# Performance work log

Measured on AMD Instinct MI355X. Metric: run time of the kernel, lower is better.

The kernel has to match this reference:

```python
import jax, jax.numpy as jnp
import numpy as np

N, E, D, H = 10000, 160000, 128, 8


def setup_inputs() -> dict:
    key = jax.random.key(0)
    ks = jax.random.split(key, 12)
    s = 0.05  # xavier-ish init scale
    return {
        "x": jax.random.normal(ks[0], (N, D), jnp.float32),
        "conn_ex": jax.random.normal(ks[1], (E, D), jnp.float32),
        "edge_index": jax.random.randint(ks[2], (2, E), 0, N),
        "sqrt_deg": jax.random.uniform(ks[3], (N, 1), jnp.float32, 0.5, 2.0),
        "qkv_w": (jax.random.normal(ks[4], (3 * D, D)) * s).astype(jnp.float32),
        "qkv_b": jnp.zeros((3 * D,), jnp.float32),
        "w1": (jax.random.normal(ks[5], (2 * D, D)) * s).astype(jnp.float32),
        "b1": jnp.zeros((2 * D,), jnp.float32),
        "wscore": (jax.random.normal(ks[6], (D // H, H, 1)) * s).astype(jnp.float32),
        "w2": (jax.random.normal(ks[7], (D, D)) * s).astype(jnp.float32),
        "b2": jnp.zeros((D,), jnp.float32),
        "bn_c_g": jnp.ones((D,), jnp.float32),
        "bn_c_b": jnp.zeros((D,), jnp.float32),
        "deg_coef": (jax.random.normal(ks[8], (1, D, 2)) * s).astype(jnp.float32),
        "ffn1_w": (jax.random.normal(ks[9], (2 * D, D)) * s).astype(jnp.float32),
        "ffn1_b": jnp.zeros((2 * D,), jnp.float32),
        "ffn2_w": (jax.random.normal(ks[10], (D, 2 * D)) * s).astype(jnp.float32),
        "ffn2_b": jnp.zeros((D,), jnp.float32),
        "bn1_g": jnp.ones((D,), jnp.float32),
        "bn1_b": jnp.zeros((D,), jnp.float32),
        "bn2_g": jnp.ones((D,), jnp.float32),
        "bn2_b": jnp.zeros((D,), jnp.float32),
        "num_nodes": N,
    }


def _bn(v, g, b):
    # BatchNorm1d, training-mode statistics (biased variance), eps=1e-5
    mu = v.mean(0)
    var = v.var(0)
    return (v - mu) / jnp.sqrt(var + 1e-5) * g + b


def _seg_softmax(s, idx, n):
    # sparse softmax over segments of dim 0 given by idx (pyg_softmax)
    m = jax.ops.segment_max(s, idx, num_segments=n)
    e = jnp.exp(s - m[idx])
    den = jax.ops.segment_sum(e, idx, num_segments=n)[idx] + 1e-16
    return e / den


def reference(x, conn_ex, edge_index, sqrt_deg, qkv_w, qkv_b, w1, b1, wscore,
              w2, b2, bn_c_g, bn_c_b, deg_coef, ffn1_w, ffn1_b, ffn2_w, ffn2_b,
              bn1_g, bn1_b, bn2_g, bn2_b, num_nodes):
    n, d = x.shape
    h = wscore.shape[1]
    dh = d // h
    # packed QKV projection
    qkv = x @ qkv_w.T + qkv_b
    Q, K, V = qkv[:, :d], qkv[:, d:2 * d], qkv[:, 2 * d:]
    dst, src = edge_index[0], edge_index[1]
    e = dst.shape[0]
    # edge-conditioned weights/bias: conn_lin1 output split into (Ew, Eb)
    Eh = conn_ex @ w1.T + b1  # [E, 2d]
    Ew, Eb = Eh[:, :d], Eh[:, d:]
    c = (Q[dst] + K[src]) * Ew
    # sqrt(relu(c)) - sqrt(relu(-c)) == sign(c)*sqrt(|c|) (signed sqrt)
    c = jnp.sign(c) * jnp.sqrt(jnp.abs(c)) + Eb
    c = jax.nn.relu(c)  # act; dropout p=0
    c2 = jax.nn.relu(_bn(c @ w2.T + b2 + conn_ex, bn_c_g, bn_c_b))  # [E, d]
    # attention scores per head
    score = jnp.einsum('ehd,dhc->ehc', c.reshape(e, h, dh), wscore)  # [E,H,1]
    score = jnp.clip(score, -5.0, 5.0)
    alpha = _seg_softmax(score, dst, num_nodes)  # [E,H,1]
    # scatter-add aggregation of weighted V and conn features
    nagg = jax.ops.segment_sum(V[src].reshape(e, h, dh) * alpha, dst, num_segments=num_nodes)
    cagg = jax.ops.segment_sum(c2.reshape(e, h, dh) * alpha, dst, num_segments=num_nodes)
    nh = (nagg + cagg).reshape(n, d)
    # degree rescaling
    nh = (jnp.stack([nh, nh * sqrt_deg], axis=-1) * deg_coef).sum(-1)
    h_res = nh + x
    nh = _bn(h_res, bn1_g, bn1_b)
    nh = jax.nn.relu(nh @ ffn1_w.T + ffn1_b) @ ffn2_w.T + ffn2_b
    nh = _bn(nh + h_res, bn2_g, bn2_b)
    return nh, c2
```

## Files before the change

### kernel.cpp

```cpp
#include <hip/hip_runtime.h>
#include <math.h>

typedef float f4 __attribute__((ext_vector_type(4)));
typedef float f2 __attribute__((ext_vector_type(2)));
typedef short bf16x8 __attribute__((ext_vector_type(8)));
typedef float f32x4v __attribute__((ext_vector_type(4)));
typedef unsigned short u16x4 __attribute__((ext_vector_type(4)));

#define N_NODES 10000
#define N_EDGES 160000

#define OFF_DEN     0
#define OFF_SUMS    80000
#define OFF_DEG     80768
#define ZERO_WORDS  90768
#define OFF_ROWPTR  90768
#define OFF_CURSOR  100772
#define OFF_ELIST   110772
#define OFF_SS      270772
#define OFF_QKV     271544
#define OFF_ESC     4111544
#define OFF_HRES    5391544
#define OFF_Y       6671544
#define OFF_MID     7951544
#define OFF_WBF     10511544

__device__ __forceinline__ unsigned short f2bf(float f) {
  unsigned int u = __float_as_uint(f);
  u = (u + 0x7fffu + ((u >> 16) & 1u)) >> 16;
  return (unsigned short)u;
}
__device__ __forceinline__ float bf2f(unsigned short p) {
  return __uint_as_float(((unsigned int)p) << 16);
}

__global__ void k_cvt(const float* __restrict__ w1, const float* __restrict__ w2,
                      unsigned short* __restrict__ w1bf,
                      unsigned short* __restrict__ w2bf) {
  int i = blockIdx.x * 256 + threadIdx.x;
  if (i < 32768) w1bf[i] = f2bf(w1[i]);
  if (i < 16384) w2bf[i] = f2bf(w2[i]);
}

__global__ __launch_bounds__(256, 4) void k_edge(
    const float* __restrict__ conn, const int* __restrict__ ei,
    const float* __restrict__ qkv, const unsigned short* __restrict__ w1bf,
    const unsigned short* __restrict__ w2bf, const float* __restrict__ b1,
    const float* __restrict__ b2, const float* __restrict__ wsc_g,
    float* __restrict__ t_out, float* __restrict__ escore,
    float* __restrict__ den, float* __restrict__ bnc_sums) {
  __shared__ unsigned short connBF[8192];
  __shared__ unsigned short qkcBF[8192];
  __shared__ float scoreAcc[64][8];
  __shared__ float wscS[128];
  __shared__ float csum[128], csq[128];
  const int tid = threadIdx.x;
  const int e0 = blockIdx.x * 64;

  if (tid < 128) { wscS[tid] = wsc_g[tid]; csum[tid] = 0.f; }
  else { csq[tid - 128] = 0.f; }

#pragma unroll
  for (int it = 0; it < 8; ++it) {
    int i = tid + it * 256;
    int row = i >> 5, kq = i & 31;
    int wb = ((row * 256 + kq * 8) ^ ((row & 7) << 4)) >> 1;
    f4 cv = *(const f4*)&conn[(e0 + row) * 128 + kq * 4];
    u16x4 cp = { f2bf(cv[0]), f2bf(cv[1]), f2bf(cv[2]), f2bf(cv[3]) };
    *(u16x4*)&connBF[wb] = cp;
    int dst = ei[e0 + row], src = ei[N_EDGES + e0 + row];
    f4 qv = *(const f4*)&qkv[dst * 384 + kq * 4];
    f4 kv = *(const f4*)&qkv[src * 384 + 128 + kq * 4];
    f4 s = qv + kv;
    u16x4 sp = { f2bf(s[0]), f2bf(s[1]), f2bf(s[2]), f2bf(s[3]) };
    *(u16x4*)&qkcBF[wb] = sp;
  }
  __syncthreads();

  const int w = tid >> 6;
  const int lq = (tid >> 4) & 3;
  const int lr = tid & 15;

  f32x4v accW[2][4] = {};
  f32x4v accB[2][4] = {};
#pragma unroll
  for (int ks = 0; ks < 4; ++ks) {
    bf16x8 a[4];
#pragma unroll
    for (int rf = 0; rf < 4; ++rf) {
      int row = rf * 16 + lr;
      int off = ((row * 256 + ks * 64 + lq * 16) ^ ((row & 7) << 4)) >> 1;
      a[rf] = *(const bf16x8*)&connBF[off];
    }
#pragma unroll
    for (int cf = 0; cf < 2; ++cf) {
      int colW = w * 32 + cf * 16 + lr;
      bf16x8 bW = *(const bf16x8*)&w1bf[colW * 128 + ks * 32 + lq * 8];
      bf16x8 bB = *(const bf16x8*)&w1bf[(128 + colW) * 128 + ks * 32 + lq * 8];
#pragma unroll
      for (int rf = 0; rf < 4; ++rf) {
        accW[cf][rf] =
            __builtin_amdgcn_mfma_f32_16x16x32_bf16(a[rf], bW, accW[cf][rf], 0, 0, 0);
        accB[cf][rf] =
            __builtin_amdgcn_mfma_f32_16x16x32_bf16(a[rf], bB, accB[cf][rf], 0, 0, 0);
      }
    }
  }
#pragma unroll
  for (int cf = 0; cf < 2; ++cf) {
    const int head = w * 2 + cf;
    const int col = w * 32 + cf * 16 + lr;
    const float wv = wscS[lr * 8 + head];
    const float bw = b1[col];
    const float bb = b1[128 + col];
#pragma unroll
    for (int rf = 0; rf < 4; ++rf) {
#pragma unroll
      for (int r = 0; r < 4; ++r) {
        int row = rf * 16 + lq * 4 + r;
        int qoff = ((row * 256 + col * 2) ^ ((row & 7) << 4)) >> 1;
        float qk = bf2f(qkcBF[qoff]);
        float ew = accW[cf][rf][r] + bw;
        float eb = accB[cf][rf][r] + bb;
        float z = qk * ew;
        float cval = fmaxf(copysignf(sqrtf(fabsf(z)), z) + eb, 0.f);
        float sp = cval * wv;
        sp += __shfl_xor(sp, 1);
        sp += __shfl_xor(sp, 2);
        sp += __shfl_xor(sp, 4);
        sp += __shfl_xor(sp, 8);
        if (lr == 0) scoreAcc[row][head] = sp;
        qkcBF[qoff] = f2bf(cval);
      }
    }
  }
  __syncthreads();

  f32x4v acc2[8] = {};
#pragma unroll
  for (int ks = 0; ks < 4; ++ks) {
    int row = w * 16 + lr;
    int off = ((row * 256 + ks * 64 + lq * 16) ^ ((row & 7) << 4)) >> 1;
    bf16x8 a = *(const bf16x8*)&qkcBF[off];
#pragma unroll
    for (int cf = 0; cf < 8; ++cf) {
      bf16x8 b = *(const bf16x8*)&w2bf[(cf * 16 + lr) * 128 + ks * 32 + lq * 8];
      acc2[cf] = __builtin_amdgcn_mfma_f32_16x16x32_bf16(a, b, acc2[cf], 0, 0, 0);
    }
  }
#pragma unroll
  for (int cf = 0; cf < 8; ++cf) {
    const int col = cf * 16 + lr;
    const float bias = b2[col];
    float sp = 0.f, qp = 0.f;
#pragma unroll
    for (int r = 0; r < 4; ++r) {
      int row = w * 16 + lq * 4 + r;
      int coff = ((row * 256 + col * 2) ^ ((row & 7) << 4)) >> 1;
      float cn = bf2f(connBF[coff]);
      float t = acc2[cf][r] + bias + cn;
      t_out[(e0 + row) * 128 + col] = t;
      sp += t;
      qp += t * t;
    }
    sp += __shfl_xor(sp, 16);
    sp += __shfl_xor(sp, 32);
    qp += __shfl_xor(qp, 16);
    qp += __shfl_xor(qp, 32);
    if (lq == 0) {
      atomicAdd(&csum[col], sp);
      atomicAdd(&csq[col], qp);
    }
  }
  __syncthreads();

  if (tid < 128) {
    atomicAdd(&bnc_sums[tid], csum[tid]);
    atomicAdd(&bnc_sums[128 + tid], csq[tid]);
  }
  for (int i = tid; i < 512; i += 256) {
    int row = i >> 3, h = i & 7;
    float s = fminf(fmaxf(scoreAcc[row][h], -5.f), 5.f);
    float es = expf(s);
    escore[(e0 + row) * 8 + h] = es;
    atomicAdd(&den[ei[e0 + row] * 8 + h], es);
  }
}

__device__ __forceinline__ void stage_w128(const float* __restrict__ w, int rowbase,
                                           int rowstride, int koff,
                                           float (*wT)[64], int tid) {
  for (int i = tid; i < 2048; i += 256) {
    int col = i & 63, k4 = i >> 6;
    f4 v = *(const f4*)&w[(rowbase + col) * rowstride + koff + k4 * 4];
    wT[k4 * 4 + 0][col] = v[0];
    wT[k4 * 4 + 1][col] = v[1];
    wT[k4 * 4 + 2][col] = v[2];
    wT[k4 * 4 + 3][col] = v[3];
  }
}

__device__ __forceinline__ void mm64(const float (*aS)[132], const float (*wT)[64],
                                     int tr, int tc, f4 acc[4]) {
#pragma unroll 4
  for (int k = 0; k < 128; k += 4) {
    f4 a0 = *(const f4*)&aS[tr * 4 + 0][k];
    f4 a1 = *(const f4*)&aS[tr * 4 + 1][k];
    f4 a2 = *(const f4*)&aS[tr * 4 + 2][k];
    f4 a3 = *(const f4*)&aS[tr * 4 + 3][k];
#pragma unroll
    for (int kk = 0; kk < 4; ++kk) {
      f4 b = *(const f4*)&wT[k + kk][tc * 4];
      acc[0] += a0[kk] * b;
      acc[1] += a1[kk] * b;
      acc[2] += a2[kk] * b;
      acc[3] += a3[kk] * b;
    }
  }
}

__global__ __launch_bounds__(256) void k_qkv(const float* __restrict__ x,
                                             const float* __restrict__ w,
                                             const float* __restrict__ b,
                                             float* __restrict__ out) {
  __shared__ float aS[64][132];
  __shared__ float wT[128][64];
  const int tid = threadIdx.x;
  const int r0 = blockIdx.x * 64;
  for (int i = tid; i < 2048; i += 256) {
    int row = i >> 5, kq = i & 31;
    int gr = r0 + row; if (gr > N_NODES - 1) gr = N_NODES - 1;
    *(f4*)&aS[row][kq * 4] = *(const f4*)&x[gr * 128 + kq * 4];
  }
  const int tr = tid >> 4, tc = tid & 15;
#pragma unroll 1
  for (int ch = 0; ch < 6; ++ch) {
    __syncthreads();
    stage_w128(w, ch * 64, 128, 0, wT, tid);
    __syncthreads();
    f4 acc[4] = {};
    mm64(aS, wT, tr, tc, acc);
    f4 bias = *(const f4*)&b[ch * 64 + tc * 4];
#pragma unroll
    for (int r = 0; r < 4; ++r) {
      int gr = r0 + tr * 4 + r;
      if (gr < N_NODES) {
        f4 o = acc[r] + bias;
        *(f4*)&out[gr * 384 + ch * 64 + tc * 4] = o;
      }
    }
  }
}

__global__ void k_deg(const int* __restrict__ ei, int* __restrict__ deg) {
  int e = blockIdx.x * 256 + threadIdx.x;
  if (e < N_EDGES) atomicAdd(&deg[ei[e]], 1);
}

__global__ __launch_bounds__(1024) void k_scan(const int* __restrict__ deg,
                                               int* __restrict__ rowptr,
                                               int* __restrict__ cursor) {
  __shared__ int ls[1024];
  const int t = threadIdx.x;
  const int base = t * 10;
  int s = 0;
#pragma unroll
  for (int i = 0; i < 10; ++i) {
    int idx = base + i;
    s += (idx < N_NODES) ? deg[idx] : 0;
  }
  ls[t] = s;
  __syncthreads();
  for (int off = 1; off < 1024; off <<= 1) {
    int v = (t >= off) ? ls[t - off] : 0;
    __syncthreads();
    ls[t] += v;
    __syncthreads();
  }
  int run = ls[t] - s;
#pragma unroll
  for (int i = 0; i < 10; ++i) {
    int idx = base + i;
    if (idx < N_NODES) {
      rowptr[idx] = run;
      cursor[idx] = run;
      run += deg[idx];
    }
  }
  if (t == 1023) rowptr[N_NODES] = ls[1023];
}

__global__ void k_scatter(const int* __restrict__ ei, int* __restrict__ cursor,
                          int* __restrict__ elist) {
  int e = blockIdx.x * 256 + threadIdx.x;
  if (e < N_EDGES) {
    int pos = atomicAdd(&cursor[ei[e]], 1);
    elist[pos] = e;
  }
}

__global__ void k_bnfin(const float* __restrict__ sums, const float* __restrict__ g,
                        const float* __restrict__ bta, float inv_n,
                        float* __restrict__ ss) {
  int c = threadIdx.x;
  float mu = sums[c] * inv_n;
  float var = sums[128 + c] * inv_n - mu * mu;
  float sc = g[c] / sqrtf(var + 1e-5f);
  ss[c] = sc;
  ss[128 + c] = bta[c] - mu * sc;
}

__global__ void k_bnapply(const float* __restrict__ in, const float* __restrict__ ss,
                          float* __restrict__ out, int n4, int relu) {
  int i = blockIdx.x * 256 + threadIdx.x;
  const int stride = gridDim.x * 256;
  for (; i < n4; i += stride) {
    int c = (i & 31) * 4;
    f4 v = *(const f4*)&in[i * 4];
    f4 sc = *(const f4*)&ss[c];
    f4 sh = *(const f4*)&ss[128 + c];
    v = v * sc + sh;
    if (relu) {
#pragma unroll
      for (int t = 0; t < 4; ++t) v[t] = fmaxf(v[t], 0.f);
    }
    *(f4*)&out[i * 4] = v;
  }
}

__global__ __launch_bounds__(256) void k_colstats(const float* __restrict__ src,
                                                  int nrows, float* __restrict__ out) {
  __shared__ float rs[128], rq[128];
  const int c = threadIdx.x & 127, rr = threadIdx.x >> 7;
  const int r0 = blockIdx.x * 256;
  float s = 0.f, q = 0.f;
  int rend = r0 + 256; if (rend > nrows) rend = nrows;
  for (int r = r0 + rr; r < rend; r += 2) {
    float v = src[r * 128 + c];
    s += v;
    q += v * v;
  }
  if (rr == 1) { rs[c] = s; rq[c] = q; }
  __syncthreads();
  if (rr == 0) {
    atomicAdd(&out[c], s + rs[c]);
    atomicAdd(&out[128 + c], q + rq[c]);
  }
}

__global__ __launch_bounds__(256) void k_agg(
    const int* __restrict__ rowptr, const int* __restrict__ elist,
    const int* __restrict__ ei, const float* __restrict__ escore,
    const float* __restrict__ den, float* __restrict__ t_c2,
    const float* __restrict__ qkv, const float* __restrict__ x,
    const float* __restrict__ sqrtdeg, const float* __restrict__ degc,
    const float* __restrict__ ss, float* __restrict__ hres) {
  const int sl = threadIdx.x & 31;
  const int n = blockIdx.x * 8 + (threadIdx.x >> 5);
  if (n >= N_NODES) return;
  const int c0 = sl * 4;
  const int head = sl >> 2;
  const int st = rowptr[n], en = rowptr[n + 1];
  const float invd = 1.f / (den[n * 8 + head] + 1e-16f);
  const f4 sc = *(const f4*)&ss[c0];
  const f4 sh = *(const f4*)&ss[128 + c0];
  f4 acc = {};
  for (int idx = st; idx < en; ++idx) {
    const int e = elist[idx];
    const float al = escore[e * 8 + head] * invd;
    const int src = ei[N_EDGES + e];
    f4 tv = *(const f4*)&t_c2[e * 128 + c0];
    f4 vv = *(const f4*)&qkv[src * 384 + 256 + c0];
    f4 c2v = tv * sc + sh;
#pragma unroll
    for (int t = 0; t < 4; ++t) c2v[t] = fmaxf(c2v[t], 0.f);
    *(f4*)&t_c2[e * 128 + c0] = c2v;
    acc += al * (c2v + vv);
  }
  const float sd = sqrtdeg[n];
  f4 d0 = { degc[c0 * 2], degc[c0 * 2 + 2], degc[c0 * 2 + 4], degc[c0 * 2 + 6] };
  f4 d1 = { degc[c0 * 2 + 1], degc[c0 * 2 + 3], degc[c0 * 2 + 5], degc[c0 * 2 + 7] };
  f4 xr = *(const f4*)&x[n * 128 + c0];
  f4 hr = acc * (d0 + sd * d1) + xr;
  *(f4*)&hres[n * 128 + c0] = hr;
}

__global__ __launch_bounds__(256) void k_ffn1(const float* __restrict__ hres,
                                              const float* __restrict__ ss,
                                              const float* __restrict__ w,
                                              const float* __restrict__ b,
                                              float* __restrict__ mid) {
  __shared__ float aS[64][132];
  __shared__ float wT[128][64];
  const int tid = threadIdx.x;
  const int r0 = blockIdx.x * 64;
  for (int i = tid; i < 2048; i += 256) {
    int row = i >> 5, kq = i & 31;
    int gr = r0 + row; if (gr > N_NODES - 1) gr = N_NODES - 1;
    f4 v = *(const f4*)&hres[gr * 128 + kq * 4];
    f4 sc = *(const f4*)&ss[kq * 4];
    f4 sh = *(const f4*)&ss[128 + kq * 4];
    *(f4*)&aS[row][kq * 4] = v * sc + sh;
  }
  const int tr = tid >> 4, tc = tid & 15;
#pragma unroll 1
  for (int ch = 0; ch < 4; ++ch) {
    __syncthreads();
    stage_w128(w, ch * 64, 128, 0, wT, tid);
    __syncthreads();
    f4 acc[4] = {};
    mm64(aS, wT, tr, tc, acc);
    f4 bias = *(const f4*)&b[ch * 64 + tc * 4];
#pragma unroll
    for (int r = 0; r < 4; ++r) {
      int gr = r0 + tr * 4 + r;
      if (gr < N_NODES) {
        f4 o = acc[r] + bias;
#pragma unroll
        for (int t = 0; t < 4; ++t) o[t] = fmaxf(o[t], 0.f);
        *(f4*)&mid[gr * 256 + ch * 64 + tc * 4] = o;
      }
    }
  }
}

__global__ __launch_bounds__(256) void k_ffn2(const float* __restrict__ mid,
                                              const float* __restrict__ w,
                                              const float* __restrict__ b,
                                              const float* __restrict__ hres,
                                              float* __restrict__ y) {
  __shared__ float aS[32][260];
  __shared__ float wT[128][64];
  const int tid = threadIdx.x;
  const int r0 = blockIdx.x * 32;
  for (int i = tid; i < 2048; i += 256) {
    int row = i >> 6, kq = i & 63;
    int gr = r0 + row; if (gr > N_NODES - 1) gr = N_NODES - 1;
    *(f4*)&aS[row][kq * 4] = *(const f4*)&mid[gr * 256 + kq * 4];
  }
  const int tr = tid >> 4, tc = tid & 15;
#pragma unroll 1
  for (int j = 0; j < 2; ++j) {
    f4 acc[2] = {};
#pragma unroll 1
    for (int kc = 0; kc < 2; ++kc) {
      __syncthreads();
      stage_w128(w, j * 64, 256, kc * 128, wT, tid);
      __syncthreads();
#pragma unroll 4
      for (int k = 0; k < 128; k += 4) {
        f4 a0 = *(const f4*)&aS[tr * 2 + 0][kc * 128 + k];
        f4 a1 = *(const f4*)&aS[tr * 2 + 1][kc * 128 + k];
#pragma unroll
        for (int kk = 0; kk < 4; ++kk) {
          f4 bv = *(const f4*)&wT[k + kk][tc * 4];
          acc[0] += a0[kk] * bv;
          acc[1] += a1[kk] * bv;
        }
      }
    }
    const int cg0 = j * 64 + tc * 4;
    f4 bias = *(const f4*)&b[cg0];
#pragma unroll
    for (int r = 0; r < 2; ++r) {
      int gr = r0 + tr * 2 + r;
      if (gr < N_NODES) {
        f4 hv = *(const f4*)&hres[gr * 128 + cg0];
        f4 o = acc[r] + bias + hv;
        *(f4*)&y[gr * 128 + cg0] = o;
      }
    }
  }
}

extern "C" void kernel_launch(void* const* d_in, const int* in_sizes, int n_in,
                              void* d_out, int out_size, void* d_ws, size_t ws_size,
                              hipStream_t stream) {
  const float* x      = (const float*)d_in[0];
  const float* conn   = (const float*)d_in[1];
  const int*   ei     = (const int*)d_in[2];
  const float* sqrtdg = (const float*)d_in[3];
  const float* qkv_w  = (const float*)d_in[4];
  const float* qkv_b  = (const float*)d_in[5];
  const float* w1     = (const float*)d_in[6];
  const float* b1     = (const float*)d_in[7];
  const float* wscore = (const float*)d_in[8];
  const float* w2     = (const float*)d_in[9];
  const float* b2     = (const float*)d_in[10];
  const float* bncg   = (const float*)d_in[11];
  const float* bncb   = (const float*)d_in[12];
  const float* degc   = (const float*)d_in[13];
  const float* f1w    = (const float*)d_in[14];
  const float* f1b    = (const float*)d_in[15];
  const float* f2w    = (const float*)d_in[16];
  const float* f2b    = (const float*)d_in[17];
  const float* bn1g   = (const float*)d_in[18];
  const float* bn1b   = (const float*)d_in[19];
  const float* bn2g   = (const float*)d_in[20];
  const float* bn2b   = (const float*)d_in[21];

  float* ws  = (float*)d_ws;
  int*   wsi = (int*)d_ws;
  float* outF = (float*)d_out;
  float* t_c2 = outF + N_NODES * 128;
  unsigned short* w1bf = (unsigned short*)(wsi + OFF_WBF);
  unsigned short* w2bf = (unsigned short*)(wsi + OFF_WBF + 16384);

  (void)hipMemsetAsync(d_ws, 0, (size_t)ZERO_WORDS * 4, stream);

  k_cvt<<<dim3(128), dim3(256), 0, stream>>>(w1, w2, w1bf, w2bf);
  k_qkv<<<dim3(157), dim3(256), 0, stream>>>(x, qkv_w, qkv_b, ws + OFF_QKV);
  k_deg<<<dim3(625), dim3(256), 0, stream>>>(ei, wsi + OFF_DEG);
  k_edge<<<dim3(2500), dim3(256), 0, stream>>>(conn, ei, ws + OFF_QKV, w1bf, w2bf,
                                               b1, b2, wscore, t_c2,
                                               ws + OFF_ESC, ws + OFF_DEN,
                                               ws + OFF_SUMS);
  k_scan<<<dim3(1), dim3(1024), 0, stream>>>(wsi + OFF_DEG, wsi + OFF_ROWPTR,
                                             wsi + OFF_CURSOR);
  k_scatter<<<dim3(625), dim3(256), 0, stream>>>(ei, wsi + OFF_CURSOR, wsi + OFF_ELIST);
  k_bnfin<<<dim3(1), dim3(128), 0, stream>>>(ws + OFF_SUMS, bncg, bncb,
                                             1.f / N_EDGES, ws + OFF_SS);
  k_agg<<<dim3(1250), dim3(256), 0, stream>>>(wsi + OFF_ROWPTR, wsi + OFF_ELIST, ei,
                                              ws + OFF_ESC, ws + OFF_DEN, t_c2,
                                              ws + OFF_QKV, x, sqrtdg, degc,
                                              ws + OFF_SS, ws + OFF_HRES);
  k_colstats<<<dim3(40), dim3(256), 0, stream>>>(ws + OFF_HRES, N_NODES,
                                                 ws + OFF_SUMS + 256);
  k_bnfin<<<dim3(1), dim3(128), 0, stream>>>(ws + OFF_SUMS + 256, bn1g, bn1b,
                                             1.f / N_NODES, ws + OFF_SS + 256);
  k_ffn1<<<dim3(157), dim3(256), 0, stream>>>(ws + OFF_HRES, ws + OFF_SS + 256,
                                              f1w, f1b, ws + OFF_MID);
  k_ffn2<<<dim3(313), dim3(256), 0, stream>>>(ws + OFF_MID, f2w, f2b, ws + OFF_HRES,
                                              ws + OFF_Y);
  k_colstats<<<dim3(40), dim3(256), 0, stream>>>(ws + OFF_Y, N_NODES,
                                                 ws + OFF_SUMS + 512);
  k_bnfin<<<dim3(1), dim3(128), 0, stream>>>(ws + OFF_SUMS + 512, bn2g, bn2b,
                                             1.f / N_NODES, ws + OFF_SS + 512);
  k_bnapply<<<dim3(1250), dim3(256), 0, stream>>>(ws + OFF_Y, ws + OFF_SS + 512,
                                                  outF, N_NODES * 128 / 4, 0);
}
```

Before: 566.3 us.

## Move node GEMMs to bf16 MFMA, prestage conn in bf16, fuse stats and launches

Converts conn_ex and all weight matrices to bf16 in one prep kernel that also counts degrees. The QKV, FFN1 and FFN2 GEMMs move from fp32 FMA to bf16 MFMA, and the BN column statistics are fused into the agg and FFN2 epilogues, which removes the colstats kernels. k_edge now runs 512 threads and reads bf16 conn from global memory instead of converting it in LDS, and it does exp and the den atomics inline. The scan gets a warp-shuffle version merged with the first BN finalize, and the final BN is applied in place on the output. This cuts kernel count and fp32 ALU work, at the cost of an extra full pass writing bf16 conn and lower precision in the node GEMMs.

```diff
diff --git a/kernel.cpp b/kernel.cpp
--- a/kernel.cpp
+++ b/kernel.cpp
@@ -18,12 +18,12 @@
 #define OFF_CURSOR  100772
 #define OFF_ELIST   110772
 #define OFF_SS      270772
-#define OFF_QKV     271544
-#define OFF_ESC     4111544
-#define OFF_HRES    5391544
-#define OFF_Y       6671544
-#define OFF_MID     7951544
-#define OFF_WBF     10511544
+#define OFF_WBF     271544
+#define OFF_QKV     353464
+#define OFF_ESC     4193464
+#define OFF_HRES    5473464
+#define OFF_MID     6753464
+#define OFF_CONNB   9313464
 
 __device__ __forceinline__ unsigned short f2bf(float f) {
   unsigned int u = __float_as_uint(f);
@@ -34,94 +34,97 @@
   return __uint_as_float(((unsigned int)p) << 16);
 }
 
-__global__ void k_cvt(const float* __restrict__ w1, const float* __restrict__ w2,
-                      unsigned short* __restrict__ w1bf,
-                      unsigned short* __restrict__ w2bf) {
-  int i = blockIdx.x * 256 + threadIdx.x;
-  if (i < 32768) w1bf[i] = f2bf(w1[i]);
-  if (i < 16384) w2bf[i] = f2bf(w2[i]);
-}
-
-__global__ __launch_bounds__(256, 4) void k_edge(
-    const float* __restrict__ conn, const int* __restrict__ ei,
+__global__ void k_prep(const float* __restrict__ conn, const float* __restrict__ w1,
+                       const float* __restrict__ w2, const float* __restrict__ qw,
+                       const float* __restrict__ f1w, const float* __restrict__ f2w,
+                       const int* __restrict__ ei, unsigned short* __restrict__ connB,
+                       unsigned short* __restrict__ wb16, int* __restrict__ deg) {
+  int g = blockIdx.x * 256 + threadIdx.x;
+  if (g < 2560000) {
+    int i0 = g * 8;
+    f4 a = *(const f4*)&conn[i0];
+    f4 b = *(const f4*)&conn[i0 + 4];
+    u16x4 pa = { f2bf(a[0]), f2bf(a[1]), f2bf(a[2]), f2bf(a[3]) };
+    u16x4 pb = { f2bf(b[0]), f2bf(b[1]), f2bf(b[2]), f2bf(b[3]) };
+    *(u16x4*)&connB[i0] = pa;
+    *(u16x4*)&connB[i0 + 4] = pb;
+  }
+  if (g < 20480) {
+    int i0 = g * 8;
+    const float* src; unsigned short* dst; int off;
+    if (i0 < 32768)       { src = w1;  dst = wb16;          off = i0; }
+    else if (i0 < 49152)  { src = w2;  dst = wb16 + 32768;  off = i0 - 32768; }
+    else if (i0 < 98304)  { src = qw;  dst = wb16 + 49152;  off = i0 - 49152; }
+    else if (i0 < 131072) { src = f1w; dst = wb16 + 98304;  off = i0 - 98304; }
+    else                  { src = f2w; dst = wb16 + 131072; off = i0 - 131072; }
+    f4 a = *(const f4*)&src[off];
+    f4 b = *(const f4*)&src[off + 4];
+    u16x4 pa = { f2bf(a[0]), f2bf(a[1]), f2bf(a[2]), f2bf(a[3]) };
+    u16x4 pb = { f2bf(b[0]), f2bf(b[1]), f2bf(b[2]), f2bf(b[3]) };
+    *(u16x4*)&dst[off] = pa;
+    *(u16x4*)&dst[off + 4] = pb;
+  }
+  if (g < N_EDGES) atomicAdd(&deg[ei[g]], 1);
+}
+
+__global__ __launch_bounds__(512, 6) void k_edge(
+    const unsigned short* __restrict__ connB, const int* __restrict__ ei,
     const float* __restrict__ qkv, const unsigned short* __restrict__ w1bf,
     const unsigned short* __restrict__ w2bf, const float* __restrict__ b1,
     const float* __restrict__ b2, const float* __restrict__ wsc_g,
     float* __restrict__ t_out, float* __restrict__ escore,
     float* __restrict__ den, float* __restrict__ bnc_sums) {
-  __shared__ unsigned short connBF[8192];
   __shared__ unsigned short qkcBF[8192];
-  __shared__ float scoreAcc[64][8];
-  __shared__ float wscS[128];
   __shared__ float csum[128], csq[128];
   const int tid = threadIdx.x;
   const int e0 = blockIdx.x * 64;
-
-  if (tid < 128) { wscS[tid] = wsc_g[tid]; csum[tid] = 0.f; }
-  else { csq[tid - 128] = 0.f; }
-
-#pragma unroll
-  for (int it = 0; it < 8; ++it) {
-    int i = tid + it * 256;
+  if (tid < 128) csum[tid] = 0.f;
+  else if (tid < 256) csq[tid - 128] = 0.f;
+
+#pragma unroll
+  for (int it = 0; it < 4; ++it) {
+    int i = tid + it * 512;
     int row = i >> 5, kq = i & 31;
-    int wb = ((row * 256 + kq * 8) ^ ((row & 7) << 4)) >> 1;
-    f4 cv = *(const f4*)&conn[(e0 + row) * 128 + kq * 4];
-    u16x4 cp = { f2bf(cv[0]), f2bf(cv[1]), f2bf(cv[2]), f2bf(cv[3]) };
-    *(u16x4*)&connBF[wb] = cp;
     int dst = ei[e0 + row], src = ei[N_EDGES + e0 + row];
     f4 qv = *(const f4*)&qkv[dst * 384 + kq * 4];
     f4 kv = *(const f4*)&qkv[src * 384 + 128 + kq * 4];
     f4 s = qv + kv;
     u16x4 sp = { f2bf(s[0]), f2bf(s[1]), f2bf(s[2]), f2bf(s[3]) };
+    int wb = ((row * 256 + kq * 8) ^ ((row & 7) << 4)) >> 1;
     *(u16x4*)&qkcBF[wb] = sp;
   }
-  __syncthreads();
 
   const int w = tid >> 6;
   const int lq = (tid >> 4) & 3;
   const int lr = tid & 15;
 
-  f32x4v accW[2][4] = {};
-  f32x4v accB[2][4] = {};
+  f32x4v accW[4] = {}, accB[4] = {};
 #pragma unroll
   for (int ks = 0; ks < 4; ++ks) {
-    bf16x8 a[4];
+    bf16x8 bW = *(const bf16x8*)&w1bf[(w * 16 + lr) * 128 + ks * 32 + lq * 8];
+    bf16x8 bB = *(const bf16x8*)&w1bf[(128 + w * 16 + lr) * 128 + ks * 32 + lq * 8];
 #pragma unroll
     for (int rf = 0; rf < 4; ++rf) {
-      int row = rf * 16 + lr;
-      int off = ((row * 256 + ks * 64 + lq * 16) ^ ((row & 7) << 4)) >> 1;
-      a[rf] = *(const bf16x8*)&connBF[off];
-    }
-#pragma unroll
-    for (int cf = 0; cf < 2; ++cf) {
-      int colW = w * 32 + cf * 16 + lr;
-      bf16x8 bW = *(const bf16x8*)&w1bf[colW * 128 + ks * 32 + lq * 8];
-      bf16x8 bB = *(const bf16x8*)&w1bf[(128 + colW) * 128 + ks * 32 + lq * 8];
-#pragma unroll
-      for (int rf = 0; rf < 4; ++rf) {
-        accW[cf][rf] =
-            __builtin_amdgcn_mfma_f32_16x16x32_bf16(a[rf], bW, accW[cf][rf], 0, 0, 0);
-        accB[cf][rf] =
-            __builtin_amdgcn_mfma_f32_16x16x32_bf16(a[rf], bB, accB[cf][rf], 0, 0, 0);
-      }
-    }
-  }
-#pragma unroll
-  for (int cf = 0; cf < 2; ++cf) {
-    const int head = w * 2 + cf;
-    const int col = w * 32 + cf * 16 + lr;
-    const float wv = wscS[lr * 8 + head];
-    const float bw = b1[col];
-    const float bb = b1[128 + col];
+      bf16x8 a = *(const bf16x8*)&connB[(e0 + rf * 16 + lr) * 128 + ks * 32 + lq * 8];
+      accW[rf] = __builtin_amdgcn_mfma_f32_16x16x32_bf16(a, bW, accW[rf], 0, 0, 0);
+      accB[rf] = __builtin_amdgcn_mfma_f32_16x16x32_bf16(a, bB, accB[rf], 0, 0, 0);
+    }
+  }
+  __syncthreads();
+
+  {
+    const float wv = wsc_g[lr * 8 + w];
+    const float bw = b1[w * 16 + lr];
+    const float bb = b1[128 + w * 16 + lr];
 #pragma unroll
     for (int rf = 0; rf < 4; ++rf) {
 #pragma unroll
       for (int r = 0; r < 4; ++r) {
         int row = rf * 16 + lq * 4 + r;
-        int qoff = ((row * 256 + col * 2) ^ ((row & 7) << 4)) >> 1;
+        int qoff = ((row * 256 + (w * 16 + lr) * 2) ^ ((row & 7) << 4)) >> 1;
         float qk = bf2f(qkcBF[qoff]);
-        float ew = accW[cf][rf][r] + bw;
-        float eb = accB[cf][rf][r] + bb;
+        float ew = accW[rf][r] + bw;
+        float eb = accB[rf][r] + bb;
         float z = qk * ew;
         float cval = fmaxf(copysignf(sqrtf(fabsf(z)), z) + eb, 0.f);
         float sp = cval * wv;
@@ -129,35 +132,41 @@
         sp += __shfl_xor(sp, 2);
         sp += __shfl_xor(sp, 4);
         sp += __shfl_xor(sp, 8);
-        if (lr == 0) scoreAcc[row][head] = sp;
+        if (lr == 0) {
+          float s = fminf(fmaxf(sp, -5.f), 5.f);
+          float es = expf(s);
+          escore[(e0 + row) * 8 + w] = es;
+          atomicAdd(&den[ei[e0 + row] * 8 + w], es);
+        }
         qkcBF[qoff] = f2bf(cval);
       }
     }
   }
   __syncthreads();
 
-  f32x4v acc2[8] = {};
+  const int r16 = (w & 3) * 16;
+  const int cb = (w >> 2) * 64;
+  f32x4v acc2[4] = {};
 #pragma unroll
   for (int ks = 0; ks < 4; ++ks) {
-    int row = w * 16 + lr;
+    int row = r16 + lr;
     int off = ((row * 256 + ks * 64 + lq * 16) ^ ((row & 7) << 4)) >> 1;
     bf16x8 a = *(const bf16x8*)&qkcBF[off];
 #pragma unroll
-    for (int cf = 0; cf < 8; ++cf) {
-      bf16x8 b = *(const bf16x8*)&w2bf[(cf * 16 + lr) * 128 + ks * 32 + lq * 8];
+    for (int cf = 0; cf < 4; ++cf) {
+      bf16x8 b = *(const bf16x8*)&w2bf[(cb + cf * 16 + lr) * 128 + ks * 32 + lq * 8];
       acc2[cf] = __builtin_amdgcn_mfma_f32_16x16x32_bf16(a, b, acc2[cf], 0, 0, 0);
     }
   }
 #pragma unroll
-  for (int cf = 0; cf < 8; ++cf) {
-    const int col = cf * 16 + lr;
+  for (int cf = 0; cf < 4; ++cf) {
+    const int col = cb + cf * 16 + lr;
     const float bias = b2[col];
     float sp = 0.f, qp = 0.f;
 #pragma unroll
     for (int r = 0; r < 4; ++r) {
-      int row = w * 16 + lq * 4 + r;
-      int coff = ((row * 256 + col * 2) ^ ((row & 7) << 4)) >> 1;
-      float cn = bf2f(connBF[coff]);
+      int row = r16 + lq * 4 + r;
+      float cn = bf2f(connB[(e0 + row) * 128 + col]);
       float t = acc2[cf][r] + bias + cn;
       t_out[(e0 + row) * 128 + col] = t;
       sp += t;
@@ -173,121 +182,121 @@
     }
   }
   __syncthreads();
-
   if (tid < 128) {
     atomicAdd(&bnc_sums[tid], csum[tid]);
     atomicAdd(&bnc_sums[128 + tid], csq[tid]);
   }
-  for (int i = tid; i < 512; i += 256) {
-    int row = i >> 3, h = i & 7;
-    float s = fminf(fmaxf(scoreAcc[row][h], -5.f), 5.f);
-    float es = expf(s);
-    escore[(e0 + row) * 8 + h] = es;
-    atomicAdd(&den[ei[e0 + row] * 8 + h], es);
-  }
-}
-
-__device__ __forceinline__ void stage_w128(const float* __restrict__ w, int rowbase,
-                                           int rowstride, int koff,
-                                           float (*wT)[64], int tid) {
-  for (int i = tid; i < 2048; i += 256) {
-    int col = i & 63, k4 = i >> 6;
-    f4 v = *(const f4*)&w[(rowbase + col) * rowstride + koff + k4 * 4];
-    wT[k4 * 4 + 0][col] = v[0];
-    wT[k4 * 4 + 1][col] = v[1];
-    wT[k4 * 4 + 2][col] = v[2];
-    wT[k4 * 4 + 3][col] = v[3];
-  }
-}
-
-__device__ __forceinline__ void mm64(const float (*aS)[132], const float (*wT)[64],
-                                     int tr, int tc, f4 acc[4]) {
-#pragma unroll 4
-  for (int k = 0; k < 128; k += 4) {
-    f4 a0 = *(const f4*)&aS[tr * 4 + 0][k];
-    f4 a1 = *(const f4*)&aS[tr * 4 + 1][k];
-    f4 a2 = *(const f4*)&aS[tr * 4 + 2][k];
-    f4 a3 = *(const f4*)&aS[tr * 4 + 3][k];
-#pragma unroll
-    for (int kk = 0; kk < 4; ++kk) {
-      f4 b = *(const f4*)&wT[k + kk][tc * 4];
-      acc[0] += a0[kk] * b;
-      acc[1] += a1[kk] * b;
-      acc[2] += a2[kk] * b;
-      acc[3] += a3[kk] * b;
-    }
-  }
-}
-
-__global__ __launch_bounds__(256) void k_qkv(const float* __restrict__ x,
-                                             const float* __restrict__ w,
-                                             const float* __restrict__ b,
-                                             float* __restrict__ out) {
-  __shared__ float aS[64][132];
-  __shared__ float wT[128][64];
+}
+
+__global__ __launch_bounds__(256, 6) void k_qkv(const float* __restrict__ x,
+                                                const unsigned short* __restrict__ qwbf,
+                                                const float* __restrict__ b,
+                                                float* __restrict__ out) {
+  __shared__ unsigned short xBF[4096];
   const int tid = threadIdx.x;
-  const int r0 = blockIdx.x * 64;
-  for (int i = tid; i < 2048; i += 256) {
+  const int r0 = blockIdx.x * 32;
+#pragma unroll
+  for (int it = 0; it < 4; ++it) {
+    int i = tid + it * 256;
     int row = i >> 5, kq = i & 31;
     int gr = r0 + row; if (gr > N_NODES - 1) gr = N_NODES - 1;
-    *(f4*)&aS[row][kq * 4] = *(const f4*)&x[gr * 128 + kq * 4];
-  }
-  const int tr = tid >> 4, tc = tid & 15;
-#pragma unroll 1
-  for (int ch = 0; ch < 6; ++ch) {
-    __syncthreads();
-    stage_w128(w, ch * 64, 128, 0, wT, tid);
-    __syncthreads();
-    f4 acc[4] = {};
-    mm64(aS, wT, tr, tc, acc);
-    f4 bias = *(const f4*)&b[ch * 64 + tc * 4];
-#pragma unroll
-    for (int r = 0; r < 4; ++r) {
-      int gr = r0 + tr * 4 + r;
-      if (gr < N_NODES) {
-        f4 o = acc[r] + bias;
-        *(f4*)&out[gr * 384 + ch * 64 + tc * 4] = o;
+    f4 v = *(const f4*)&x[gr * 128 + kq * 4];
+    u16x4 p = { f2bf(v[0]), f2bf(v[1]), f2bf(v[2]), f2bf(v[3]) };
+    int wb = ((row * 256 + kq * 8) ^ ((row & 7) << 4)) >> 1;
+    *(u16x4*)&xBF[wb] = p;
+  }
+  __syncthreads();
+  const int w = tid >> 6, lq = (tid >> 4) & 3, lr = tid & 15;
+  f32x4v acc[2][6] = {};
+#pragma unroll
+  for (int ks = 0; ks < 4; ++ks) {
+    bf16x8 a0, a1;
+    {
+      int row = lr;
+      a0 = *(const bf16x8*)&xBF[((row * 256 + ks * 64 + lq * 16) ^ ((row & 7) << 4)) >> 1];
+      row = 16 + lr;
+      a1 = *(const bf16x8*)&xBF[((row * 256 + ks * 64 + lq * 16) ^ ((row & 7) << 4)) >> 1];
+    }
+#pragma unroll
+    for (int cf = 0; cf < 6; ++cf) {
+      bf16x8 bv = *(const bf16x8*)&qwbf[(w * 96 + cf * 16 + lr) * 128 + ks * 32 + lq * 8];
+      acc[0][cf] = __builtin_amdgcn_mfma_f32_16x16x32_bf16(a0, bv, acc[0][cf], 0, 0, 0);
+      acc[1][cf] = __builtin_amdgcn_mfma_f32_16x16x32_bf16(a1, bv, acc[1][cf], 0, 0, 0);
+    }
+  }
+#pragma unroll
+  for (int rf = 0; rf < 2; ++rf) {
+#pragma unroll
+    for (int cf = 0; cf < 6; ++cf) {
+      int col = w * 96 + cf * 16 + lr;
+      float bias = b[col];
+#pragma unroll
+      for (int r = 0; r < 4; ++r) {
+        int gr = r0 + rf * 16 + lq * 4 + r;
+        if (gr < N_NODES) out[gr * 384 + col] = acc[rf][cf][r] + bias;
       }
     }
   }
 }
 
-__global__ void k_deg(const int* __restrict__ ei, int* __restrict__ deg) {
-  int e = blockIdx.x * 256 + threadIdx.x;
-  if (e < N_EDGES) atomicAdd(&deg[ei[e]], 1);
-}
-
-__global__ __launch_bounds__(1024) void k_scan(const int* __restrict__ deg,
-                                               int* __restrict__ rowptr,
-                                               int* __restrict__ cursor) {
-  __shared__ int ls[1024];
+__global__ __launch_bounds__(1024) void k_scanfin(
+    const int* __restrict__ deg, int* __restrict__ rowptr, int* __restrict__ cursor,
+    const float* __restrict__ sums, const float* __restrict__ g,
+    const float* __restrict__ bta, float* __restrict__ ss) {
+  if (blockIdx.x == 1) {
+    int c = threadIdx.x;
+    if (c < 128) {
+      float inv_n = 1.f / N_EDGES;
+      float mu = sums[c] * inv_n;
+      float var = sums[128 + c] * inv_n - mu * mu;
+      float sc = g[c] / sqrtf(var + 1e-5f);
+      ss[c] = sc;
+      ss[128 + c] = bta[c] - mu * sc;
+    }
+    return;
+  }
+  __shared__ int wsum[16];
   const int t = threadIdx.x;
   const int base = t * 10;
-  int s = 0;
+  int d[10];
+  int s0 = 0;
 #pragma unroll
   for (int i = 0; i < 10; ++i) {
     int idx = base + i;
-    s += (idx < N_NODES) ? deg[idx] : 0;
-  }
-  ls[t] = s;
-  __syncthreads();
-  for (int off = 1; off < 1024; off <<= 1) {
-    int v = (t >= off) ? ls[t - off] : 0;
-    __syncthreads();
-    ls[t] += v;
-    __syncthreads();
-  }
-  int run = ls[t] - s;
+    d[i] = (idx < N_NODES) ? deg[idx] : 0;
+    s0 += d[i];
+  }
+  int s = s0;
+  const int lane = t & 63;
+#pragma unroll
+  for (int o = 1; o < 64; o <<= 1) {
+    int v = __shfl_up(s, o);
+    if (lane >= o) s += v;
+  }
+  if (lane == 63) wsum[t >> 6] = s;
+  __syncthreads();
+  if (t < 16) {
+    int v = wsum[t];
+#pragma unroll
+    for (int o = 1; o < 16; o <<= 1) {
+      int u = __shfl_up(v, o);
+      if (t >= o) v += u;
+    }
+    wsum[t] = v;
+  }
+  __syncthreads();
+  int incl = s + ((t >= 64) ? wsum[(t >> 6) - 1] : 0);
+  int run = incl - s0;
 #pragma unroll
   for (int i = 0; i < 10; ++i) {
     int idx = base + i;
     if (idx < N_NODES) {
       rowptr[idx] = run;
       cursor[idx] = run;
-      run += deg[idx];
-    }
-  }
-  if (t == 1023) rowptr[N_NODES] = ls[1023];
+      run += d[i];
+    }
+  }
+  if (t == 1023) rowptr[N_NODES] = incl;
 }
 
 __global__ void k_scatter(const int* __restrict__ ei, int* __restrict__ cursor,
@@ -310,54 +319,21 @@
   ss[128 + c] = bta[c] - mu * sc;
 }
 
-__global__ void k_bnapply(const float* __restrict__ in, const float* __restrict__ ss,
-                          float* __restrict__ out, int n4, int relu) {
-  int i = blockIdx.x * 256 + threadIdx.x;
-  const int stride = gridDim.x * 256;
-  for (; i < n4; i += stride) {
-    int c = (i & 31) * 4;
-    f4 v = *(const f4*)&in[i * 4];
-    f4 sc = *(const f4*)&ss[c];
-    f4 sh = *(const f4*)&ss[128 + c];
-    v = v * sc + sh;
-    if (relu) {
-#pragma unroll
-      for (int t = 0; t < 4; ++t) v[t] = fmaxf(v[t], 0.f);
-    }
-    *(f4*)&out[i * 4] = v;
-  }
-}
-
-__global__ __launch_bounds__(256) void k_colstats(const float* __restrict__ src,
-                                                  int nrows, float* __restrict__ out) {
-  __shared__ float rs[128], rq[128];
-  const int c = threadIdx.x & 127, rr = threadIdx.x >> 7;
-  const int r0 = blockIdx.x * 256;
-  float s = 0.f, q = 0.f;
-  int rend = r0 + 256; if (rend > nrows) rend = nrows;
-  for (int r = r0 + rr; r < rend; r += 2) {
-    float v = src[r * 128 + c];
-    s += v;
-    q += v * v;
-  }
-  if (rr == 1) { rs[c] = s; rq[c] = q; }
-  __syncthreads();
-  if (rr == 0) {
-    atomicAdd(&out[c], s + rs[c]);
-    atomicAdd(&out[128 + c], q + rq[c]);
-  }
-}
-
 __global__ __launch_bounds__(256) void k_agg(
     const int* __restrict__ rowptr, const int* __restrict__ elist,
     const int* __restrict__ ei, const float* __restrict__ escore,
     const float* __restrict__ den, float* __restrict__ t_c2,
     const float* __restrict__ qkv, const float* __restrict__ x,
     const float* __restrict__ sqrtdeg, const float* __restrict__ degc,
-    const float* __restrict__ ss, float* __restrict__ hres) {
-  const int sl = threadIdx.x & 31;
-  const int n = blockIdx.x * 8 + (threadIdx.x >> 5);
-  if (n >= N_NODES) return;
+    const float* __restrict__ ss, float* __restrict__ hres,
+    float* __restrict__ bn1_sums) {
+  __shared__ float csum[128], csq[128];
+  const int tid = threadIdx.x;
+  if (tid < 128) csum[tid] = 0.f;
+  else csq[tid - 128] = 0.f;
+  __syncthreads();
+  const int sl = tid & 31;
+  const int n = blockIdx.x * 8 + (tid >> 5);
   const int c0 = sl * 4;
   const int head = sl >> 2;
   const int st = rowptr[n], en = rowptr[n + 1];
@@ -365,16 +341,18 @@
   const f4 sc = *(const f4*)&ss[c0];
   const f4 sh = *(const f4*)&ss[128 + c0];
   f4 acc = {};
+  int e = (st < en) ? elist[st] : 0;
   for (int idx = st; idx < en; ++idx) {
-    const int e = elist[idx];
-    const float al = escore[e * 8 + head] * invd;
-    const int src = ei[N_EDGES + e];
-    f4 tv = *(const f4*)&t_c2[e * 128 + c0];
+    const int ec = e;
+    if (idx + 1 < en) e = elist[idx + 1];
+    const float al = escore[ec * 8 + head] * invd;
+    const int src = ei[N_EDGES + ec];
+    f4 tv = *(const f4*)&t_c2[ec * 128 + c0];
     f4 vv = *(const f4*)&qkv[src * 384 + 256 + c0];
     f4 c2v = tv * sc + sh;
 #pragma unroll
     for (int t = 0; t < 4; ++t) c2v[t] = fmaxf(c2v[t], 0.f);
-    *(f4*)&t_c2[e * 128 + c0] = c2v;
+    *(f4*)&t_c2[ec * 128 + c0] = c2v;
     acc += al * (c2v + vv);
   }
   const float sd = sqrtdeg[n];
@@ -383,93 +361,151 @@
   f4 xr = *(const f4*)&x[n * 128 + c0];
   f4 hr = acc * (d0 + sd * d1) + xr;
   *(f4*)&hres[n * 128 + c0] = hr;
-}
-
-__global__ __launch_bounds__(256) void k_ffn1(const float* __restrict__ hres,
-                                              const float* __restrict__ ss,
-                                              const float* __restrict__ w,
-                                              const float* __restrict__ b,
-                                              float* __restrict__ mid) {
-  __shared__ float aS[64][132];
-  __shared__ float wT[128][64];
+#pragma unroll
+  for (int t = 0; t < 4; ++t) {
+    atomicAdd(&csum[c0 + t], hr[t]);
+    atomicAdd(&csq[c0 + t], hr[t] * hr[t]);
+  }
+  __syncthreads();
+  if (tid < 128) {
+    atomicAdd(&bn1_sums[tid], csum[tid]);
+    atomicAdd(&bn1_sums[128 + tid], csq[tid]);
+  }
+}
+
+__global__ __launch_bounds__(256, 6) void k_ffn1(const float* __restrict__ hres,
+                                                 const float* __restrict__ ss,
+                                                 const unsigned short* __restrict__ wbf,
+                                                 const float* __restrict__ b,
+                                                 float* __restrict__ mid) {
+  __shared__ unsigned short aBF[4096];
   const int tid = threadIdx.x;
-  const int r0 = blockIdx.x * 64;
-  for (int i = tid; i < 2048; i += 256) {
+  const int r0 = blockIdx.x * 32;
+#pragma unroll
+  for (int it = 0; it < 4; ++it) {
+    int i = tid + it * 256;
     int row = i >> 5, kq = i & 31;
     int gr = r0 + row; if (gr > N_NODES - 1) gr = N_NODES - 1;
     f4 v = *(const f4*)&hres[gr * 128 + kq * 4];
     f4 sc = *(const f4*)&ss[kq * 4];
     f4 sh = *(const f4*)&ss[128 + kq * 4];
-    *(f4*)&aS[row][kq * 4] = v * sc + sh;
-  }
-  const int tr = tid >> 4, tc = tid & 15;
-#pragma unroll 1
-  for (int ch = 0; ch < 4; ++ch) {
-    __syncthreads();
-    stage_w128(w, ch * 64, 128, 0, wT, tid);
-    __syncthreads();
-    f4 acc[4] = {};
-    mm64(aS, wT, tr, tc, acc);
-    f4 bias = *(const f4*)&b[ch * 64 + tc * 4];
-#pragma unroll
-    for (int r = 0; r < 4; ++r) {
-      int gr = r0 + tr * 4 + r;
-      if (gr < N_NODES) {
-        f4 o = acc[r] + bias;
-#pragma unroll
-        for (int t = 0; t < 4; ++t) o[t] = fmaxf(o[t], 0.f);
-        *(f4*)&mid[gr * 256 + ch * 64 + tc * 4] = o;
+    v = v * sc + sh;
+    u16x4 p = { f2bf(v[0]), f2bf(v[1]), f2bf(v[2]), f2bf(v[3]) };
+    int wb = ((row * 256 + kq * 8) ^ ((row & 7) << 4)) >> 1;
+    *(u16x4*)&aBF[wb] = p;
+  }
+  __syncthreads();
+  const int w = tid >> 6, lq = (tid >> 4) & 3, lr = tid & 15;
+  f32x4v acc[2][4] = {};
+#pragma unroll
+  for (int ks = 0; ks < 4; ++ks) {
+    bf16x8 a0, a1;
+    {
+      int row = lr;
+      a0 = *(const bf16x8*)&aBF[((row * 256 + ks * 64 + lq * 16) ^ ((row & 7) << 4)) >> 1];
+      row = 16 + lr;
+      a1 = *(const bf16x8*)&aBF[((row * 256 + ks * 64 + lq * 16) ^ ((row & 7) << 4)) >> 1];
+    }
+#pragma unroll
+    for (int cf = 0; cf < 4; ++cf) {
+      bf16x8 bv = *(const bf16x8*)&wbf[(w * 64 + cf * 16 + lr) * 128 + ks * 32 + lq * 8];
+      acc[0][cf] = __builtin_amdgcn_mfma_f32_16x16x32_bf16(a0, bv, acc[0][cf], 0, 0, 0);
+      acc[1][cf] = __builtin_amdgcn_mfma_f32_16x16x32_bf16(a1, bv, acc[1][cf], 0, 0, 0);
+    }
+  }
+#pragma unroll
+  for (int rf = 0; rf < 2; ++rf) {
+#pragma unroll
+    for (int cf = 0; cf < 4; ++cf) {
+      int col = w * 64 + cf * 16 + lr;
+      float bias = b[col];
+#pragma unroll
+      for (int r = 0; r < 4; ++r) {
+        int gr = r0 + rf * 16 + lq * 4 + r;
+        if (gr < N_NODES) mid[gr * 256 + col] = fmaxf(acc[rf][cf][r] + bias, 0.f);
       }
     }
   }
 }
 
-__global__ __launch_bounds__(256) void k_ffn2(const float* __restrict__ mid,
-                                              const float* __restrict__ w,
-                                              const float* __restrict__ b,
-                                              const float* __restrict__ hres,
-                                              float* __restrict__ y) {
-  __shared__ float aS[32][260];
-  __shared__ float wT[128][64];
+__global__ __launch_bounds__(256, 6) void k_ffn2(const float* __restrict__ mid,
+                                                 const unsigned short* __restrict__ wbf,
+                                                 const float* __restrict__ b,
+                                                 const float* __restrict__ hres,
+                                                 float* __restrict__ y,
+                                                 float* __restrict__ bn2_sums) {
+  __shared__ unsigned short aBF[8192];
+  __shared__ float csum[128], csq[128];
   const int tid = threadIdx.x;
   const int r0 = blockIdx.x * 32;
-  for (int i = tid; i < 2048; i += 256) {
+  if (tid < 128) csum[tid] = 0.f;
+  else csq[tid - 128] = 0.f;
+#pragma unroll
+  for (int it = 0; it < 8; ++it) {
+    int i = tid + it * 256;
     int row = i >> 6, kq = i & 63;
     int gr = r0 + row; if (gr > N_NODES - 1) gr = N_NODES - 1;
-    *(f4*)&aS[row][kq * 4] = *(const f4*)&mid[gr * 256 + kq * 4];
-  }
-  const int tr = tid >> 4, tc = tid & 15;
-#pragma unroll 1
-  for (int j = 0; j < 2; ++j) {
-    f4 acc[2] = {};
-#pragma unroll 1
-    for (int kc = 0; kc < 2; ++kc) {
-      __syncthreads();
-      stage_w128(w, j * 64, 256, kc * 128, wT, tid);
-      __syncthreads();
-#pragma unroll 4
-      for (int k = 0; k < 128; k += 4) {
-        f4 a0 = *(const f4*)&aS[tr * 2 + 0][kc * 128 + k];
-        f4 a1 = *(const f4*)&aS[tr * 2 + 1][kc * 128 + k];
-#pragma unroll
-        for (int kk = 0; kk < 4; ++kk) {
-          f4 bv = *(const f4*)&wT[k + kk][tc * 4];
-          acc[0] += a0[kk] * bv;
-          acc[1] += a1[kk] * bv;
+    f4 v = *(const f4*)&mid[gr * 256 + kq * 4];
+    u16x4 p = { f2bf(v[0]), f2bf(v[1]), f2bf(v[2]), f2bf(v[3]) };
+    int wb = ((row * 512 + kq * 8) ^ ((row & 7) << 4)) >> 1;
+    *(u16x4*)&aBF[wb] = p;
+  }
+  __syncthreads();
+  const int w = tid >> 6, lq = (tid >> 4) & 3, lr = tid & 15;
+  f32x4v acc[2][2] = {};
+#pragma unroll
+  for (int ks = 0; ks < 8; ++ks) {
+    bf16x8 a0, a1;
+    {
+      int row = lr;
+      a0 = *(const bf16x8*)&aBF[((row * 512 + ks * 64 + lq * 16) ^ ((row & 7) << 4)) >> 1];
+      row = 16 + lr;
+      a1 = *(const bf16x8*)&aBF[((row * 512 + ks * 64 + lq * 16) ^ ((row & 7) << 4)) >> 1];
+    }
+#pragma unroll
+    for (int cf = 0; cf < 2; ++cf) {
+      bf16x8 bv = *(const bf16x8*)&wbf[(w * 32 + cf * 16 + lr) * 256 + ks * 32 + lq * 8];
+      acc[0][cf] = __builtin_amdgcn_mfma_f32_16x16x32_bf16(a0, bv, acc[0][cf], 0, 0, 0);
+      acc[1][cf] = __builtin_amdgcn_mfma_f32_16x16x32_bf16(a1, bv, acc[1][cf], 0, 0, 0);
+    }
+  }
+#pragma unroll
+  for (int rf = 0; rf < 2; ++rf) {
+#pragma unroll
+    for (int cf = 0; cf < 2; ++cf) {
+      int col = w * 32 + cf * 16 + lr;
+      float bias = b[col];
+      float sp = 0.f, qp = 0.f;
+#pragma unroll
+      for (int r = 0; r < 4; ++r) {
+        int gr = r0 + rf * 16 + lq * 4 + r;
+        if (gr < N_NODES) {
+          float o = acc[rf][cf][r] + bias + hres[gr * 128 + col];
+          y[gr * 128 + col] = o;
+          sp += o;
+          qp += o * o;
         }
       }
-    }
-    const int cg0 = j * 64 + tc * 4;
-    f4 bias = *(const f4*)&b[cg0];
-#pragma unroll
-    for (int r = 0; r < 2; ++r) {
-      int gr = r0 + tr * 2 + r;
-      if (gr < N_NODES) {
-        f4 hv = *(const f4*)&hres[gr * 128 + cg0];
-        f4 o = acc[r] + bias + hv;
-        *(f4*)&y[gr * 128 + cg0] = o;
-      }
-    }
+      atomicAdd(&csum[col], sp);
+      atomicAdd(&csq[col], qp);
+    }
+  }
+  __syncthreads();
+  if (tid < 128) {
+    atomicAdd(&bn2_sums[tid], csum[tid]);
+    atomicAdd(&bn2_sums[128 + tid], csq[tid]);
+  }
+}
+
+__global__ void k_bnfinal(float* __restrict__ yio, const float* __restrict__ ss) {
+  int i = blockIdx.x * 256 + threadIdx.x;
+  if (i < N_NODES * 32) {
+    int c = (i & 31) * 4;
+    f4 v = *(const f4*)&yio[i * 4];
+    f4 sc = *(const f4*)&ss[c];
+    f4 sh = *(const f4*)&ss[128 + c];
+    v = v * sc + sh;
+    *(f4*)&yio[i * 4] = v;
   }
 }
 
@@ -503,39 +539,39 @@
   int*   wsi = (int*)d_ws;
   float* outF = (float*)d_out;
   float* t_c2 = outF + N_NODES * 128;
-  unsigned short* w1bf = (unsigned short*)(wsi + OFF_WBF);
-  unsigned short* w2bf = (unsigned short*)(wsi + OFF_WBF + 16384);
+  unsigned short* connB = (unsigned short*)(wsi + OFF_CONNB);
+  unsigned short* wb16  = (unsigned short*)(wsi + OFF_WBF);
+  unsigned short* w1bf  = wb16;
+  unsigned short* w2bf  = wb16 + 32768;
+  unsigned short* qwbf  = wb16 + 49152;
+  unsigned short* f1wbf = wb16 + 98304;
+  unsigned short* f2wbf = wb16 + 131072;
 
   (void)hipMemsetAsync(d_ws, 0, (size_t)ZERO_WORDS * 4, stream);
 
-  k_cvt<<<dim3(128), dim3(256), 0, stream>>>(w1, w2, w1bf, w2bf);
-  k_qkv<<<dim3(157), dim3(256), 0, stream>>>(x, qkv_w, qkv_b, ws + OFF_QKV);
-  k_deg<<<dim3(625), dim3(256), 0, stream>>>(ei, wsi + OFF_DEG);
-  k_edge<<<dim3(2500), dim3(256), 0, stream>>>(conn, ei, ws + OFF_QKV, w1bf, w2bf,
+  k_prep<<<dim3(10000), dim3(256), 0, stream>>>(conn, w1, w2, qkv_w, f1w, f2w, ei,
+                                                connB, wb16, wsi + OFF_DEG);
+  k_qkv<<<dim3(313), dim3(256), 0, stream>>>(x, qwbf, qkv_b, ws + OFF_QKV);
+  k_edge<<<dim3(2500), dim3(512), 0, stream>>>(connB, ei, ws + OFF_QKV, w1bf, w2bf,
                                                b1, b2, wscore, t_c2,
                                                ws + OFF_ESC, ws + OFF_DEN,
                                                ws + OFF_SUMS);
-  k_scan<<<dim3(1), dim3(1024), 0, stream>>>(wsi + OFF_DEG, wsi + OFF_ROWPTR,
-                                             wsi + OFF_CURSOR);
+  k_scanfin<<<dim3(2), dim3(1024), 0, stream>>>(wsi + OFF_DEG, wsi + OFF_ROWPTR,
+                                                wsi + OFF_CURSOR, ws + OFF_SUMS,
+                                                bncg, bncb, ws + OFF_SS);
   k_scatter<<<dim3(625), dim3(256), 0, stream>>>(ei, wsi + OFF_CURSOR, wsi + OFF_ELIST);
-  k_bnfin<<<dim3(1), dim3(128), 0, stream>>>(ws + OFF_SUMS, bncg, bncb,
-                                             1.f / N_EDGES, ws + OFF_SS);
   k_agg<<<dim3(1250), dim3(256), 0, stream>>>(wsi + OFF_ROWPTR, wsi + OFF_ELIST, ei,
                                               ws + OFF_ESC, ws + OFF_DEN, t_c2,
                                               ws + OFF_QKV, x, sqrtdg, degc,
-                                              ws + OFF_SS, ws + OFF_HRES);
-  k_colstats<<<dim3(40), dim3(256), 0, stream>>>(ws + OFF_HRES, N_NODES,
-                                                 ws + OFF_SUMS + 256);
+                                              ws + OFF_SS, ws + OFF_HRES,
+                                              ws + OFF_SUMS + 256);
   k_bnfin<<<dim3(1), dim3(128), 0, stream>>>(ws + OFF_SUMS + 256, bn1g, bn1b,
                                              1.f / N_NODES, ws + OFF_SS + 256);
-  k_ffn1<<<dim3(157), dim3(256), 0, stream>>>(ws + OFF_HRES, ws + OFF_SS + 256,
-                                              f1w, f1b, ws + OFF_MID);
-  k_ffn2<<<dim3(313), dim3(256), 0, stream>>>(ws + OFF_MID, f2w, f2b, ws + OFF_HRES,
-                                              ws + OFF_Y);
-  k_colstats<<<dim3(40), dim3(256), 0, stream>>>(ws + OFF_Y, N_NODES,
-                                                 ws + OFF_SUMS + 512);
+  k_ffn1<<<dim3(313), dim3(256), 0, stream>>>(ws + OFF_HRES, ws + OFF_SS + 256,
+                                              f1wbf, f1b, ws + OFF_MID);
+  k_ffn2<<<dim3(313), dim3(256), 0, stream>>>(ws + OFF_MID, f2wbf, f2b, ws + OFF_HRES,
+                                              outF, ws + OFF_SUMS + 512);
   k_bnfin<<<dim3(1), dim3(128), 0, stream>>>(ws + OFF_SUMS + 512, bn2g, bn2b,
                                              1.f / N_NODES, ws + OFF_SS + 512);
-  k_bnapply<<<dim3(1250), dim3(256), 0, stream>>>(ws + OFF_Y, ws + OFF_SS + 512,
-                                                  outF, N_NODES * 128 / 4, 0);
-}
+  k_bnfinal<<<dim3(1250), dim3(256), 0, stream>>>(outF, ws + OFF_SS + 512);
+}
```

Result: faster. 511.2 us (-9.7%).
